# Performance work log

Hardware: AMD Instinct MI355X
Metric: run time of the kernel (lower is better)

Reference implementation:

```python
import jax, jax.numpy as jnp
import numpy as np

FEAT = 128
N_RBF = 20
CUTOFF = 5.0
N_GRAPHS = 128
ATOMS = 64
N_ATOMS = N_GRAPHS * ATOMS  # 8192
N_EDGES = N_ATOMS * 32      # 262144


def setup_inputs() -> dict:
    key = jax.random.key(0)
    ks = jax.random.split(key, 12)
    s_j = jax.random.normal(ks[0], (N_ATOMS, FEAT), jnp.float32)
    v_j = jax.random.normal(ks[1], (N_ATOMS, FEAT, 3), jnp.float32)
    r_ij = jax.random.normal(ks[2], (N_EDGES, 3), jnp.float32) * 1.5
    nbrs = jax.random.randint(ks[3], (N_EDGES, 2), 0, N_ATOMS, dtype=jnp.int32)
    num_atoms = jnp.full((N_GRAPHS,), ATOMS, dtype=jnp.int32)
    sc = 0.05
    W1 = jax.random.normal(ks[4], (FEAT, FEAT), jnp.float32) * sc
    b1 = jnp.zeros((FEAT,), jnp.float32)
    W2 = jax.random.normal(ks[5], (FEAT, 3 * FEAT), jnp.float32) * sc
    b2 = jnp.zeros((3 * FEAT,), jnp.float32)
    Wr = jax.random.normal(ks[6], (N_RBF, 3 * FEAT), jnp.float32) * sc
    br = jnp.zeros((3 * FEAT,), jnp.float32)
    Wd = jax.random.normal(ks[7], (FEAT, 3 * FEAT), jnp.float32) * sc
    bd = jnp.zeros((3 * FEAT,), jnp.float32)
    return {"s_j": s_j, "v_j": v_j, "r_ij": r_ij, "nbrs": nbrs,
            "num_atoms": num_atoms, "W1": W1, "b1": b1, "W2": W2, "b2": b2,
            "Wr": Wr, "br": br, "Wd": Wd, "bd": bd}


def _forward(s_j, v_j, r_ij, nbrs, W1, b1, W2, b2, Wr, br, Wd, bd):
    # preprocess_r
    dist = jnp.linalg.norm(r_ij, axis=-1)            # [E]
    unit = r_ij / dist[:, None]                      # [E,3]

    # InvariantMessage: per-atom MLP, gather at nbrs[:,1], times radial filter
    phi = jax.nn.silu(s_j @ W1 + b1) @ W2 + b2       # [N, 3F]
    phi_e = phi[nbrs[:, 1]]                          # [E, 3F]
    n = jnp.arange(1, N_RBF + 1, dtype=jnp.float32)
    rbf = jnp.sin(n[None, :] * jnp.pi * dist[:, None] / CUTOFF) / dist[:, None]  # [E, n_rbf]
    env = jnp.where(dist < CUTOFF, 0.5 * (jnp.cos(jnp.pi * dist / CUTOFF) + 1.0), 0.0)
    w_s = (rbf @ Wr + br) * env[:, None]             # [E, 3F]
    inv_out = (phi_e * w_s).reshape(-1, 3, FEAT)     # [E, 3, F]

    split_0 = inv_out[:, 0, :][..., None]            # [E, F, 1]
    split_1 = inv_out[:, 1, :]                       # [E, F]
    split_2 = inv_out[:, 2, :][..., None]            # [E, F, 1]

    unit_add = split_2 * unit[:, None, :]            # [E, F, 3]
    delta_v_ij = unit_add + split_0 * v_j[nbrs[:, 1]]  # [E, F, 3]
    delta_s_ij = split_1                             # [E, F]

    seg = nbrs[:, 0]
    delta_v_i = jax.ops.segment_sum(delta_v_ij, seg, num_segments=N_ATOMS)
    delta_s_l = jax.ops.segment_sum(delta_s_ij, seg, num_segments=N_ATOMS)

    # NonLocalInteraction: per-graph exact softmax attention (uniform graph size)
    qkv = s_j @ Wd + bd                              # [N, 3F]
    Q, K, V = jnp.split(qkv, 3, axis=-1)
    Qb = Q.reshape(N_GRAPHS, ATOMS, FEAT)
    Kb = K.reshape(N_GRAPHS, ATOMS, FEAT)
    Vb = V.reshape(N_GRAPHS, ATOMS, FEAT)
    scores = jnp.einsum('bqf,bkf->bqk', Qb, Kb) / jnp.sqrt(jnp.float32(FEAT))
    att = jnp.einsum('bqk,bkf->bqf', jax.nn.softmax(scores, axis=-1), Vb)
    delta_s_nl = att.reshape(N_ATOMS, FEAT)

    delta_s_i = delta_s_l + delta_s_nl
    return delta_s_i, delta_v_i


def reference(s_j, v_j, r_ij, nbrs, num_atoms, W1, b1, W2, b2, Wr, br, Wd, bd):
    # num_atoms is uniform (ATOMS per graph); attention is batched accordingly.
    return _forward(s_j, v_j, r_ij, nbrs, W1, b1, W2, b2, Wr, br, Wd, bd)
```

## Files before the change

kernel.cpp:

```cpp
#include <hip/hip_runtime.h>
#include <hip/hip_bf16.h>
#include <cstdint>

#define FEAT    128
#define NRBF    20
#define NATOMS  8192
#define NEDGES  262144
#define NGRAPH  128
#define APG     64
#define PI_F    3.14159265358979323846f
#define CUTOFF_F 5.0f
#define QTUS    ((size_t)NATOMS * 32 * 6)
#define APW     8

typedef unsigned int uint_t;
typedef unsigned short ushort_t;
typedef __attribute__((ext_vector_type(4))) float f32x4;
typedef __attribute__((ext_vector_type(4))) short short4v;
typedef __attribute__((ext_vector_type(8))) short short8;
struct U3 { uint_t x, y, z; };

__device__ __forceinline__ float bflo(uint_t u) { return __uint_as_float(u << 16); }
__device__ __forceinline__ float bfhi(uint_t u) { return __uint_as_float(u & 0xffff0000u); }
__device__ __forceinline__ float bfus(ushort_t u) { return __uint_as_float((uint_t)u << 16); }
__device__ __forceinline__ ushort_t f2bf(float f) {
  uint_t u = __float_as_uint(f);
  return (ushort_t)((u + 0x7fffu + ((u >> 16) & 1u)) >> 16);
}
__device__ __forceinline__ uint_t pack2(float lo, float hi) {
  return (uint_t)f2bf(lo) | ((uint_t)f2bf(hi) << 16);
}

__device__ __forceinline__ ushort_t swz_elem(const float* __restrict__ W, int N,
                                             int NT, int i) {
  int jj = i & 7, lane = (i >> 3) & 63, tile = i >> 9;
  int ks = tile / NT, ctg = tile - ks * NT;
  int g = lane >> 4, q = lane & 15;
  int k = 32 * ks + 4 * g + (jj & 3) + 16 * (jj >> 2);
  int c = 16 * ctg + q;
  return f2bf(W[(size_t)k * N + c]);
}

__global__ void prep_kernel(const float* __restrict__ v_j, const float* __restrict__ W1,
                            const float* __restrict__ W2, const float* __restrict__ Wd,
                            const float* __restrict__ Wr, const float* __restrict__ br,
                            ushort_t* __restrict__ PV, ushort_t* __restrict__ w1s,
                            ushort_t* __restrict__ w2s, ushort_t* __restrict__ wds,
                            ushort_t* __restrict__ wrs) {
  int i = blockIdx.x * 256 + threadIdx.x;
  if (i < NATOMS * FEAT) {
    int j = i >> 7, f = i & 127;
    int tbl = f >> 5, fl = f & 31;
    const float* vp = v_j + (size_t)i * 3;
    uint_t* o = reinterpret_cast<uint_t*>(PV + (size_t)tbl * QTUS + ((size_t)j * 32 + fl) * 6);
    o[0] = 0u;
    o[1] = pack2(0.f, vp[0]);
    o[2] = pack2(vp[1], vp[2]);
    return;
  }
  i -= NATOMS * FEAT;
  if (i < 16384) { w1s[i] = swz_elem(W1, 128, 8, i); return; }
  i -= 16384;
  if (i < 49152) { w2s[i] = swz_elem(W2, 384, 24, i); return; }
  i -= 49152;
  if (i < 49152) { wds[i] = swz_elem(Wd, 384, 24, i); return; }
  i -= 49152;
  if (i < 12288) {
    int jj = i & 7, lane = (i >> 3) & 63, ct = i >> 9;
    int g = lane >> 4, q = lane & 15;
    int k = 4 * g + (jj & 3) + 16 * (jj >> 2);
    int f = 16 * ct + q;
    float v = (k < NRBF) ? Wr[k * 384 + f] : (k == NRBF ? br[f] : 0.f);
    wrs[i] = f2bf(v);
  }
}

__global__ __launch_bounds__(256) void gemm_fused12(
    const float* __restrict__ s_j, const ushort_t* __restrict__ w1s,
    const float* __restrict__ b1, const ushort_t* __restrict__ w2s,
    const float* __restrict__ b2, ushort_t* __restrict__ PV) {
  __shared__ ushort_t As[64][136];
  __shared__ ushort_t Hs[64][136];
  const int t = threadIdx.x;
  const int r0 = blockIdx.x * 64;
  const int w = t >> 6, l = t & 63, g = l >> 4, q = l & 15;

  for (int i = t; i < 64 * 32; i += 256) {
    int r = i >> 5, k4 = i & 31;
    float4 v = *reinterpret_cast<const float4*>(s_j + (size_t)(r0 + r) * 128 + 4 * k4);
    ushort4 o = {f2bf(v.x), f2bf(v.y), f2bf(v.z), f2bf(v.w)};
    *reinterpret_cast<ushort4*>(&As[r][4 * k4]) = o;
  }
  __syncthreads();

  short8 afr[4];
  #pragma unroll
  for (int ks = 0; ks < 4; ++ks) {
    const ushort_t* ap = &As[16 * w + q][32 * ks + 4 * g];
    short4v alo = *reinterpret_cast<const short4v*>(ap);
    short4v ahi = *reinterpret_cast<const short4v*>(ap + 16);
    afr[ks] = short8{alo[0], alo[1], alo[2], alo[3], ahi[0], ahi[1], ahi[2], ahi[3]};
  }
  #pragma unroll
  for (int ct = 0; ct < 8; ++ct) {
    f32x4 acc = {};
    #pragma unroll
    for (int ks = 0; ks < 4; ++ks) {
      short8 bf = *reinterpret_cast<const short8*>(
          w1s + ((size_t)(ks * 8 + ct) * 64 + l) * 8);
      acc = __builtin_amdgcn_mfma_f32_16x16x32_bf16(afr[ks], bf, acc, 0, 0, 0);
    }
    float bb = b1[16 * ct + q];
    #pragma unroll
    for (int r = 0; r < 4; ++r) {
      float o = acc[r] + bb;
      o = o / (1.f + __expf(-o));
      Hs[16 * w + 4 * g + r][16 * ct + q] = f2bf(o);
    }
  }
  __syncthreads();

  short8 hfr[4];
  #pragma unroll
  for (int ks = 0; ks < 4; ++ks) {
    const ushort_t* ap = &Hs[16 * w + q][32 * ks + 4 * g];
    short4v alo = *reinterpret_cast<const short4v*>(ap);
    short4v ahi = *reinterpret_cast<const short4v*>(ap + 16);
    hfr[ks] = short8{alo[0], alo[1], alo[2], alo[3], ahi[0], ahi[1], ahi[2], ahi[3]};
  }
  for (int cb = 0; cb < 6; ++cb) {
    #pragma unroll
    for (int ct = 0; ct < 4; ++ct) {
      f32x4 acc = {};
      #pragma unroll
      for (int ks = 0; ks < 4; ++ks) {
        short8 bf = *reinterpret_cast<const short8*>(
            w2s + ((size_t)(ks * 24 + cb * 4 + ct) * 64 + l) * 8);
        acc = __builtin_amdgcn_mfma_f32_16x16x32_bf16(hfr[ks], bf, acc, 0, 0, 0);
      }
      int col = cb * 64 + 16 * ct + q;
      float bb = b2[col];
      int f = col & 127, s = col >> 7;
      int tbl = f >> 5, fl = f & 31;
      #pragma unroll
      for (int r = 0; r < 4; ++r) {
        float o = acc[r] + bb;
        int row = r0 + 16 * w + 4 * g + r;
        PV[(size_t)tbl * QTUS + ((size_t)row * 32 + fl) * 6 + s] = f2bf(o);
      }
    }
  }
}

__global__ __launch_bounds__(256) void gemm_mfma(
    const void* __restrict__ Asrc, int a_f32, const ushort_t* __restrict__ Wswz,
    const float* __restrict__ bias, int N, int NT, int silu, int omode,
    void* __restrict__ p0, void* __restrict__ p1) {
  __shared__ ushort_t As[64][136];
  const int t = threadIdx.x;
  const int r0 = blockIdx.x * 64, c0 = blockIdx.y * 64;
  const int w = t >> 6, l = t & 63, g = l >> 4, q = l & 15;

  short8 bf[4][4];
  #pragma unroll
  for (int ks = 0; ks < 4; ++ks)
    #pragma unroll
    for (int ct = 0; ct < 4; ++ct)
      bf[ks][ct] = *reinterpret_cast<const short8*>(
          Wswz + ((size_t)(ks * NT + (c0 >> 4) + ct) * 64 + l) * 8);

  if (a_f32) {
    const float* Af = (const float*)Asrc;
    for (int i = t; i < 64 * 32; i += 256) {
      int r = i >> 5, k4 = i & 31;
      float4 v = *reinterpret_cast<const float4*>(Af + (size_t)(r0 + r) * 128 + 4 * k4);
      ushort4 o = {f2bf(v.x), f2bf(v.y), f2bf(v.z), f2bf(v.w)};
      *reinterpret_cast<ushort4*>(&As[r][4 * k4]) = o;
    }
  } else {
    const ushort_t* Ab = (const ushort_t*)Asrc;
    for (int i = t; i < 64 * 16; i += 256) {
      int r = i >> 4, g8 = i & 15;
      short8 v = *reinterpret_cast<const short8*>(Ab + (size_t)(r0 + r) * 128 + 8 * g8);
      *reinterpret_cast<short8*>(&As[r][8 * g8]) = v;
    }
  }
  __syncthreads();

  f32x4 acc[4] = {};
  #pragma unroll
  for (int ks = 0; ks < 4; ++ks) {
    const ushort_t* ap = &As[16 * w + q][32 * ks + 4 * g];
    short4v alo = *reinterpret_cast<const short4v*>(ap);
    short4v ahi = *reinterpret_cast<const short4v*>(ap + 16);
    short8 af;
    af[0] = alo[0]; af[1] = alo[1]; af[2] = alo[2]; af[3] = alo[3];
    af[4] = ahi[0]; af[5] = ahi[1]; af[6] = ahi[2]; af[7] = ahi[3];
    #pragma unroll
    for (int ct = 0; ct < 4; ++ct)
      acc[ct] = __builtin_amdgcn_mfma_f32_16x16x32_bf16(af, bf[ks][ct], acc[ct], 0, 0, 0);
  }

  #pragma unroll
  for (int ct = 0; ct < 4; ++ct) {
    int col = c0 + 16 * ct + q;
    float bb = bias[col];
    #pragma unroll
    for (int r = 0; r < 4; ++r) {
      float o = acc[ct][r] + bb;
      if (silu) o = o / (1.f + __expf(-o));
      int row = r0 + 16 * w + 4 * g + r;
      if (omode == 1) {
        ((ushort_t*)p0)[(size_t)row * N + col] = f2bf(o);
      } else {
        if (col < 128) ((float*)p0)[(size_t)row * 128 + col] = o;
        else           ((ushort_t*)p1)[(size_t)row * 256 + col - 128] = f2bf(o);
      }
    }
  }
}

__global__ void hist_kernel(const int* __restrict__ nbrs, int* __restrict__ counts) {
  int e = blockIdx.x * blockDim.x + threadIdx.x;
  if (e < NEDGES) atomicAdd(&counts[nbrs[2 * e]], 1);
}

__global__ __launch_bounds__(1024) void scan_kernel(
    const int* __restrict__ counts, int* __restrict__ offs, int* __restrict__ cursor) {
  __shared__ int part[1024];
  const int t = threadIdx.x;
  int local[8];
  int s = 0;
  #pragma unroll
  for (int i = 0; i < 8; ++i) { local[i] = counts[t * 8 + i]; s += local[i]; }
  part[t] = s;
  __syncthreads();
  for (int off = 1; off < 1024; off <<= 1) {
    int v = part[t];
    int add = (t >= off) ? part[t - off] : 0;
    __syncthreads();
    part[t] = v + add;
    __syncthreads();
  }
  int excl = part[t] - s;
  #pragma unroll
  for (int i = 0; i < 8; ++i) {
    offs[t * 8 + i] = excl;
    cursor[t * 8 + i] = excl;
    excl += local[i];
  }
  if (t == 1023) offs[NATOMS] = excl;
}

__global__ void scatter_kernel(const int* __restrict__ nbrs, const float* __restrict__ r_ij,
                               int* __restrict__ cursor, uint4* __restrict__ erec) {
  int e = blockIdx.x * blockDim.x + threadIdx.x;
  if (e < NEDGES) {
    int2 nb = *reinterpret_cast<const int2*>(nbrs + 2 * e);
    int pos = atomicAdd(&cursor[nb.x], 1);
    const float* rp = r_ij + 3 * e;
    erec[pos] = make_uint4((uint_t)nb.y, __float_as_uint(rp[0]),
                           __float_as_uint(rp[1]), __float_as_uint(rp[2]));
  }
}

__global__ __launch_bounds__(256) void edge_mfma8(
    const uint4* __restrict__ erec, const int* __restrict__ offs,
    const ushort_t* __restrict__ PV, const ushort_t* __restrict__ wrs,
    float* __restrict__ out_s, float* __restrict__ out_v) {
  __shared__ short8 sW[6 * 64];
  const int t = threadIdx.x;
  const int qtr = blockIdx.x & 3;
  for (int i = t; i < 6 * 64; i += 256) {
    int tl = i >> 6, l2 = i & 63;
    int s = tl >> 1, c = tl & 1;
    sW[i] = *reinterpret_cast<const short8*>(
        wrs + ((size_t)(s * 8 + 2 * qtr + c) * 64 + l2) * 8);
  }
  __syncthreads();

  const int w = t >> 6, l = t & 63, g = l >> 4, q = l & 15;
  const int a0 = ((blockIdx.x >> 2) * 4 + w) * APW;
  const float c1 = PI_F / CUTOFF_F;
  const char* PVb = reinterpret_cast<const char*>(PV) + (size_t)qtr * QTUS * 2;

  int eb = offs[a0];
  int end = offs[a0 + 1];
  uint4 er = make_uint4(0u, 0u, 0u, 0u);
  if (eb + q < end) er = erec[eb + q];

  for (int aidx = 0; aidx < APW; ++aidx) {
    const int end_next = (aidx + 1 < APW) ? offs[a0 + aidx + 2] : 0;
    float ds0 = 0.f, ds1 = 0.f;
    float dv[2][3] = {};

    for (;;) {
      const bool last = (eb + 16 >= end);
      const int neb = last ? end : (eb + 16);
      const int nend = last ? ((aidx + 1 < APW) ? end_next : neb) : end;
      uint4 ern = make_uint4(0u, 0u, 0u, 0u);
      if (neb + q < nend) ern = erec[neb + q];

      float ang = 0.f, ie = 0.f, env = 0.f, u0 = 0.f, u1 = 0.f, u2 = 0.f;
      int jn = 0;
      if (eb + q < end) {
        jn = (int)er.x;
        float x = __uint_as_float(er.y), y = __uint_as_float(er.z), z = __uint_as_float(er.w);
        float d = sqrtf(x * x + y * y + z * z);
        float inv = 1.f / d;
        ang = c1 * d;
        env = (d < CUTOFF_F) ? 0.5f * (__cosf(ang) + 1.f) : 0.f;
        ie = inv * env;
        u0 = x * inv; u1 = y * inv; u2 = z * inv;
      }
      const char* pb[4];
      float ub[4][3];
      #pragma unroll
      for (int r = 0; r < 4; ++r) {
        int src = 4 * g + r;
        int jr = __shfl(jn, src, 64);
        ub[r][0] = __shfl(u0, src, 64);
        ub[r][1] = __shfl(u1, src, 64);
        ub[r][2] = __shfl(u2, src, 64);
        pb[r] = PVb + (size_t)jr * 384 + (size_t)q * 12;
      }
      U3 ld[2][4];
      #pragma unroll
      for (int c = 0; c < 2; ++c)
        #pragma unroll
        for (int r = 0; r < 4; ++r)
          ld[c][r] = *reinterpret_cast<const U3*>(pb[r] + (size_t)c * 192);
      short8 af;
      #pragma unroll
      for (int jj = 0; jj < 8; ++jj) {
        int k = 4 * g + (jj & 3) + 16 * (jj >> 2);
        float v = (k < NRBF) ? ie * __sinf((float)(k + 1) * ang)
                             : (k == NRBF ? env : 0.f);
        af[jj] = (short)f2bf(v);
      }
      #pragma unroll
      for (int c = 0; c < 2; ++c) {
        short8 b0 = sW[(0 * 2 + c) * 64 + l];
        short8 b1 = sW[(1 * 2 + c) * 64 + l];
        short8 b2 = sW[(2 * 2 + c) * 64 + l];
        f32x4 z4 = {0.f, 0.f, 0.f, 0.f};
        f32x4 cs0 = __builtin_amdgcn_mfma_f32_16x16x32_bf16(af, b0, z4, 0, 0, 0);
        f32x4 cs1 = __builtin_amdgcn_mfma_f32_16x16x32_bf16(af, b1, z4, 0, 0, 0);
        f32x4 cs2 = __builtin_amdgcn_mfma_f32_16x16x32_bf16(af, b2, z4, 0, 0, 0);
        #pragma unroll
        for (int r = 0; r < 4; ++r) {
          U3 u = ld[c][r];
          float p0 = bflo(u.x), p1 = bfhi(u.x);
          float p2 = bflo(u.y), v0 = bfhi(u.y);
          float v1 = bflo(u.z), v2 = bfhi(u.z);
          float pw0 = p0 * cs0[r];
          if (c == 0) ds0 += p1 * cs1[r]; else ds1 += p1 * cs1[r];
          float pw2 = p2 * cs2[r];
          dv[c][0] += pw0 * v0 + pw2 * ub[r][0];
          dv[c][1] += pw0 * v1 + pw2 * ub[r][1];
          dv[c][2] += pw0 * v2 + pw2 * ub[r][2];
        }
      }
      er = ern;
      eb = neb;
      if (last) break;
    }

    float r0v = ds0, r1v = ds1;
    r0v += __shfl_xor(r0v, 16, 64); r0v += __shfl_xor(r0v, 32, 64);
    r1v += __shfl_xor(r1v, 16, 64); r1v += __shfl_xor(r1v, 32, 64);
    float dvr[2][3];
    #pragma unroll
    for (int c = 0; c < 2; ++c)
      #pragma unroll
      for (int cc = 0; cc < 3; ++cc) {
        float y = dv[c][cc];
        y += __shfl_xor(y, 16, 64); y += __shfl_xor(y, 32, 64);
        dvr[c][cc] = y;
      }
    if (g < 2) {
      int atom = a0 + aidx;
      float sv = (g == 0) ? r0v : r1v;
      float d0 = (g == 0) ? dvr[0][0] : dvr[1][0];
      float d1 = (g == 0) ? dvr[0][1] : dvr[1][1];
      float d2 = (g == 0) ? dvr[0][2] : dvr[1][2];
      int f = 32 * qtr + 16 * g + q;
      out_s[(size_t)atom * FEAT + f] = sv;
      float* ov = out_v + (size_t)atom * 384 + (size_t)f * 3;
      ov[0] = d0; ov[1] = d1; ov[2] = d2;
    }
    end = end_next;
  }
}

__device__ __forceinline__ float wave_max64(float v) {
  #pragma unroll
  for (int m = 32; m > 0; m >>= 1) v = fmaxf(v, __shfl_xor(v, m, 64));
  return v;
}
__device__ __forceinline__ float wave_sum64(float v) {
  #pragma unroll
  for (int m = 32; m > 0; m >>= 1) v += __shfl_xor(v, m, 64);
  return v;
}

__global__ __launch_bounds__(256) void attn_kernel(const float* __restrict__ Qf,
                                                   const ushort_t* __restrict__ kvbf,
                                                   float* __restrict__ out_s) {
  __shared__ float4 Ks4[64 * 32];
  __shared__ float  Vs[64][130];
  __shared__ float  Ps[4][4][64];
  const int b = blockIdx.x >> 1, half = blockIdx.x & 1;
  const int t = threadIdx.x;
  const float* qbase = Qf + (size_t)b * APG * 128;
  const ushort_t* kvb = kvbf + (size_t)b * APG * 256;

  for (int i = t; i < 64 * 32; i += 256) {
    int a = i >> 5, gg = i & 31;
    ushort4 k4 = *reinterpret_cast<const ushort4*>(kvb + a * 256 + 4 * gg);
    float4 kf = {bfus(k4.x), bfus(k4.y), bfus(k4.z), bfus(k4.w)};
    Ks4[a * 32 + (gg ^ (a & 7))] = kf;
  }
  for (int i = t; i < 64 * 32; i += 256) {
    int a = i >> 5, gg = i & 31;
    ushort4 v4 = *reinterpret_cast<const ushort4*>(kvb + a * 256 + 128 + 4 * gg);
    Vs[a][4 * gg + 0] = bfus(v4.x); Vs[a][4 * gg + 1] = bfus(v4.y);
    Vs[a][4 * gg + 2] = bfus(v4.z); Vs[a][4 * gg + 3] = bfus(v4.w);
  }
  __syncthreads();

  const int w = t >> 6, l = t & 63;
  const float scale = 0.08838834764831845f;

  for (int qq = 8 * half + w; qq < 8 * half + 8; qq += 4) {
    const float* q0p = qbase + (size_t)(4 * qq + 0) * 128;
    const float* q1p = qbase + (size_t)(4 * qq + 1) * 128;
    const float* q2p = qbase + (size_t)(4 * qq + 2) * 128;
    const float* q3p = qbase + (size_t)(4 * qq + 3) * 128;
    float s0 = 0.f, s1 = 0.f, s2 = 0.f, s3 = 0.f;
    #pragma unroll 8
    for (int i = 0; i < 32; ++i) {
      float4 k = Ks4[l * 32 + (i ^ (l & 7))];
      float4 q0 = *reinterpret_cast<const float4*>(q0p + 4 * i);
      float4 q1 = *reinterpret_cast<const float4*>(q1p + 4 * i);
      float4 q2 = *reinterpret_cast<const float4*>(q2p + 4 * i);
      float4 q3 = *reinterpret_cast<const float4*>(q3p + 4 * i);
      s0 += q0.x * k.x + q0.y * k.y + q0.z * k.z + q0.w * k.w;
      s1 += q1.x * k.x + q1.y * k.y + q1.z * k.z + q1.w * k.w;
      s2 += q2.x * k.x + q2.y * k.y + q2.z * k.z + q2.w * k.w;
      s3 += q3.x * k.x + q3.y * k.y + q3.z * k.z + q3.w * k.w;
    }
    s0 *= scale; s1 *= scale; s2 *= scale; s3 *= scale;

    float p0 = __expf(s0 - wave_max64(s0));
    float p1 = __expf(s1 - wave_max64(s1));
    float p2 = __expf(s2 - wave_max64(s2));
    float p3 = __expf(s3 - wave_max64(s3));
    p0 /= wave_sum64(p0); p1 /= wave_sum64(p1);
    p2 /= wave_sum64(p2); p3 /= wave_sum64(p3);

    Ps[w][0][l] = p0; Ps[w][1][l] = p1; Ps[w][2][l] = p2; Ps[w][3][l] = p3;
    __threadfence_block();

    float a00 = 0.f, a01 = 0.f, a10 = 0.f, a11 = 0.f;
    float a20 = 0.f, a21 = 0.f, a30 = 0.f, a31 = 0.f;
    for (int a = 0; a < 64; ++a) {
      float2 v = *reinterpret_cast<const float2*>(&Vs[a][2 * l]);
      float pa0 = Ps[w][0][a], pa1 = Ps[w][1][a];
      float pa2 = Ps[w][2][a], pa3 = Ps[w][3][a];
      a00 += pa0 * v.x; a01 += pa0 * v.y;
      a10 += pa1 * v.x; a11 += pa1 * v.y;
      a20 += pa2 * v.x; a21 += pa2 * v.y;
      a30 += pa3 * v.x; a31 += pa3 * v.y;
    }
    size_t row0 = (size_t)(b * APG + 4 * qq) * FEAT + 2 * l;
    float2* o0 = reinterpret_cast<float2*>(out_s + row0);
    float2* o1 = reinterpret_cast<float2*>(out_s + row0 + FEAT);
    float2* o2 = reinterpret_cast<float2*>(out_s + row0 + 2 * FEAT);
    float2* o3 = reinterpret_cast<float2*>(out_s + row0 + 3 * FEAT);
    float2 c0 = *o0; c0.x += a00; c0.y += a01; *o0 = c0;
    float2 c1 = *o1; c1.x += a10; c1.y += a11; *o1 = c1;
    float2 c2 = *o2; c2.x += a20; c2.y += a21; *o2 = c2;
    float2 c3 = *o3; c3.x += a30; c3.y += a31; *o3 = c3;
    __threadfence_block();
  }
}

extern "C" void kernel_launch(void* const* d_in, const int* in_sizes, int n_in,
                              void* d_out, int out_size, void* d_ws, size_t ws_size,
                              hipStream_t stream) {
  const float* s_j  = (const float*)d_in[0];
  const float* v_j  = (const float*)d_in[1];
  const float* r_ij = (const float*)d_in[2];
  const int*   nbrs = (const int*)d_in[3];
  const float* W1   = (const float*)d_in[5];
  const float* b1   = (const float*)d_in[6];
  const float* W2   = (const float*)d_in[7];
  const float* b2   = (const float*)d_in[8];
  const float* Wr   = (const float*)d_in[9];
  const float* br   = (const float*)d_in[10];
  const float* Wd   = (const float*)d_in[11];
  const float* bd   = (const float*)d_in[12];

  float* out_s = (float*)d_out;
  float* out_v = out_s + (size_t)NATOMS * FEAT;

  float*    Qf   = (float*)d_ws;
  ushort_t* kvbf = (ushort_t*)(Qf + NATOMS * FEAT);
  ushort_t* PV   = kvbf + (size_t)NATOMS * 256;
  ushort_t* w1s  = PV + 4 * QTUS;
  ushort_t* w2s  = w1s + 16384;
  ushort_t* wds  = w2s + 49152;
  ushort_t* wrs  = wds + 49152;
  uint4*    erec = (uint4*)(wrs + 12288);
  int* offs   = (int*)(erec + NEDGES);
  int* cursor = offs + (NATOMS + 1);
  int* counts = cursor + NATOMS;

  int prep_total = NATOMS * FEAT + 16384 + 49152 + 49152 + 12288;
  prep_kernel<<<(prep_total + 255) / 256, 256, 0, stream>>>(
      v_j, W1, W2, Wd, Wr, br, PV, w1s, w2s, wds, wrs);

  gemm_fused12<<<NATOMS / 64, 256, 0, stream>>>(s_j, w1s, b1, w2s, b2, PV);

  hipMemsetAsync(counts, 0, NATOMS * sizeof(int), stream);
  hist_kernel<<<NEDGES / 256, 256, 0, stream>>>(nbrs, counts);
  scan_kernel<<<1, 1024, 0, stream>>>(counts, offs, cursor);
  scatter_kernel<<<NEDGES / 256, 256, 0, stream>>>(nbrs, r_ij, cursor, erec);

  gemm_mfma<<<dim3(NATOMS / 64, 6), 256, 0, stream>>>(
      s_j, 1, wds, bd, 384, 24, 0, 3, Qf, kvbf);

  edge_mfma8<<<NATOMS / APW, 256, 0, stream>>>(erec, offs, PV, wrs, out_s, out_v);
  attn_kernel<<<NGRAPH * 2, 256, 0, stream>>>(Qf, kvbf, out_s);
}
```

Measured before the change: 141.5 us.

## Merge GEMM launches, fold histogram into prep, widen grids for edge and attention

Folds the edge histogram into the prep kernel and merges the phi MLP GEMM and the QKV GEMM into one launch. In the merged launch, blocks with y<6 each compute one 64-column slice of W2 and blocks with y>=6 compute the QKV projection. Because of this split, each phi block recomputes the first-layer SiLU hidden tile, six times redundantly per row block. APW drops from 8 to 4, doubling the edge kernel's grid, and the attention grid grows to 4 blocks per graph so each wave handles one query group. The aim is fewer launches and more parallelism, paid for with duplicated first-layer GEMM work and a K/V tile reload per extra attention block.

```diff
diff --git a/kernel.cpp b/kernel.cpp
--- a/kernel.cpp
+++ b/kernel.cpp
@@ -11,7 +11,7 @@
 #define PI_F    3.14159265358979323846f
 #define CUTOFF_F 5.0f
 #define QTUS    ((size_t)NATOMS * 32 * 6)
-#define APW     8
+#define APW     4
 
 typedef unsigned int uint_t;
 typedef unsigned short ushort_t;
@@ -44,9 +44,10 @@
 __global__ void prep_kernel(const float* __restrict__ v_j, const float* __restrict__ W1,
                             const float* __restrict__ W2, const float* __restrict__ Wd,
                             const float* __restrict__ Wr, const float* __restrict__ br,
+                            const int* __restrict__ nbrs,
                             ushort_t* __restrict__ PV, ushort_t* __restrict__ w1s,
                             ushort_t* __restrict__ w2s, ushort_t* __restrict__ wds,
-                            ushort_t* __restrict__ wrs) {
+                            ushort_t* __restrict__ wrs, int* __restrict__ counts) {
   int i = blockIdx.x * 256 + threadIdx.x;
   if (i < NATOMS * FEAT) {
     int j = i >> 7, f = i & 127;
@@ -72,35 +73,66 @@
     int f = 16 * ct + q;
     float v = (k < NRBF) ? Wr[k * 384 + f] : (k == NRBF ? br[f] : 0.f);
     wrs[i] = f2bf(v);
-  }
-}
-
-__global__ __launch_bounds__(256) void gemm_fused12(
+    return;
+  }
+  i -= 12288;
+  if (i < NEDGES) atomicAdd(&counts[nbrs[2 * i]], 1);
+}
+
+__global__ __launch_bounds__(256) void gemm_big(
     const float* __restrict__ s_j, const ushort_t* __restrict__ w1s,
     const float* __restrict__ b1, const ushort_t* __restrict__ w2s,
-    const float* __restrict__ b2, ushort_t* __restrict__ PV) {
-  __shared__ ushort_t As[64][136];
-  __shared__ ushort_t Hs[64][136];
+    const float* __restrict__ b2, const ushort_t* __restrict__ wds,
+    const float* __restrict__ bd, ushort_t* __restrict__ PV,
+    float* __restrict__ Qf, ushort_t* __restrict__ kvbf) {
+  __shared__ ushort_t Buf[64][136];
   const int t = threadIdx.x;
   const int r0 = blockIdx.x * 64;
+  const int y = blockIdx.y;
   const int w = t >> 6, l = t & 63, g = l >> 4, q = l & 15;
 
   for (int i = t; i < 64 * 32; i += 256) {
     int r = i >> 5, k4 = i & 31;
     float4 v = *reinterpret_cast<const float4*>(s_j + (size_t)(r0 + r) * 128 + 4 * k4);
     ushort4 o = {f2bf(v.x), f2bf(v.y), f2bf(v.z), f2bf(v.w)};
-    *reinterpret_cast<ushort4*>(&As[r][4 * k4]) = o;
+    *reinterpret_cast<ushort4*>(&Buf[r][4 * k4]) = o;
   }
   __syncthreads();
 
   short8 afr[4];
   #pragma unroll
   for (int ks = 0; ks < 4; ++ks) {
-    const ushort_t* ap = &As[16 * w + q][32 * ks + 4 * g];
+    const ushort_t* ap = &Buf[16 * w + q][32 * ks + 4 * g];
     short4v alo = *reinterpret_cast<const short4v*>(ap);
     short4v ahi = *reinterpret_cast<const short4v*>(ap + 16);
     afr[ks] = short8{alo[0], alo[1], alo[2], alo[3], ahi[0], ahi[1], ahi[2], ahi[3]};
   }
+
+  if (y >= 6) {
+    const int yy = y - 6;
+    #pragma unroll
+    for (int ct = 0; ct < 4; ++ct) {
+      f32x4 acc = {};
+      #pragma unroll
+      for (int ks = 0; ks < 4; ++ks) {
+        short8 bf = *reinterpret_cast<const short8*>(
+            wds + ((size_t)(ks * 24 + yy * 4 + ct) * 64 + l) * 8);
+        acc = __builtin_amdgcn_mfma_f32_16x16x32_bf16(afr[ks], bf, acc, 0, 0, 0);
+      }
+      int col = yy * 64 + 16 * ct + q;
+      float bb = bd[col];
+      #pragma unroll
+      for (int r = 0; r < 4; ++r) {
+        float o = acc[r] + bb;
+        int row = r0 + 16 * w + 4 * g + r;
+        if (col < 128) Qf[(size_t)row * 128 + col] = o;
+        else           kvbf[(size_t)row * 256 + col - 128] = f2bf(o);
+      }
+    }
+    return;
+  }
+
+  __syncthreads();
   #pragma unroll
   for (int ct = 0; ct < 8; ++ct) {
     f32x4 acc = {};
@@ -115,7 +147,7 @@
     for (int r = 0; r < 4; ++r) {
       float o = acc[r] + bb;
       o = o / (1.f + __expf(-o));
-      Hs[16 * w + 4 * g + r][16 * ct + q] = f2bf(o);
+      Buf[16 * w + 4 * g + r][16 * ct + q] = f2bf(o);
     }
   }
   __syncthreads();
@@ -123,106 +155,31 @@
   short8 hfr[4];
   #pragma unroll
   for (int ks = 0; ks < 4; ++ks) {
-    const ushort_t* ap = &Hs[16 * w + q][32 * ks + 4 * g];
+    const ushort_t* ap = &Buf[16 * w + q][32 * ks + 4 * g];
     short4v alo = *reinterpret_cast<const short4v*>(ap);
     short4v ahi = *reinterpret_cast<const short4v*>(ap + 16);
     hfr[ks] = short8{alo[0], alo[1], alo[2], alo[3], ahi[0], ahi[1], ahi[2], ahi[3]};
   }
-  for (int cb = 0; cb < 6; ++cb) {
-    #pragma unroll
-    for (int ct = 0; ct < 4; ++ct) {
-      f32x4 acc = {};
-      #pragma unroll
-      for (int ks = 0; ks < 4; ++ks) {
-        short8 bf = *reinterpret_cast<const short8*>(
-            w2s + ((size_t)(ks * 24 + cb * 4 + ct) * 64 + l) * 8);
-        acc = __builtin_amdgcn_mfma_f32_16x16x32_bf16(hfr[ks], bf, acc, 0, 0, 0);
-      }
-      int col = cb * 64 + 16 * ct + q;
-      float bb = b2[col];
-      int f = col & 127, s = col >> 7;
-      int tbl = f >> 5, fl = f & 31;
-      #pragma unroll
-      for (int r = 0; r < 4; ++r) {
-        float o = acc[r] + bb;
-        int row = r0 + 16 * w + 4 * g + r;
-        PV[(size_t)tbl * QTUS + ((size_t)row * 32 + fl) * 6 + s] = f2bf(o);
-      }
-    }
-  }
-}
-
-__global__ __launch_bounds__(256) void gemm_mfma(
-    const void* __restrict__ Asrc, int a_f32, const ushort_t* __restrict__ Wswz,
-    const float* __restrict__ bias, int N, int NT, int silu, int omode,
-    void* __restrict__ p0, void* __restrict__ p1) {
-  __shared__ ushort_t As[64][136];
-  const int t = threadIdx.x;
-  const int r0 = blockIdx.x * 64, c0 = blockIdx.y * 64;
-  const int w = t >> 6, l = t & 63, g = l >> 4, q = l & 15;
-
-  short8 bf[4][4];
-  #pragma unroll
-  for (int ks = 0; ks < 4; ++ks)
-    #pragma unroll
-    for (int ct = 0; ct < 4; ++ct)
-      bf[ks][ct] = *reinterpret_cast<const short8*>(
-          Wswz + ((size_t)(ks * NT + (c0 >> 4) + ct) * 64 + l) * 8);
-
-  if (a_f32) {
-    const float* Af = (const float*)Asrc;
-    for (int i = t; i < 64 * 32; i += 256) {
-      int r = i >> 5, k4 = i & 31;
-      float4 v = *reinterpret_cast<const float4*>(Af + (size_t)(r0 + r) * 128 + 4 * k4);
-      ushort4 o = {f2bf(v.x), f2bf(v.y), f2bf(v.z), f2bf(v.w)};
-      *reinterpret_cast<ushort4*>(&As[r][4 * k4]) = o;
-    }
-  } else {
-    const ushort_t* Ab = (const ushort_t*)Asrc;
-    for (int i = t; i < 64 * 16; i += 256) {
-      int r = i >> 4, g8 = i & 15;
-      short8 v = *reinterpret_cast<const short8*>(Ab + (size_t)(r0 + r) * 128 + 8 * g8);
-      *reinterpret_cast<short8*>(&As[r][8 * g8]) = v;
-    }
-  }
-  __syncthreads();
-
-  f32x4 acc[4] = {};
-  #pragma unroll
-  for (int ks = 0; ks < 4; ++ks) {
-    const ushort_t* ap = &As[16 * w + q][32 * ks + 4 * g];
-    short4v alo = *reinterpret_cast<const short4v*>(ap);
-    short4v ahi = *reinterpret_cast<const short4v*>(ap + 16);
-    short8 af;
-    af[0] = alo[0]; af[1] = alo[1]; af[2] = alo[2]; af[3] = alo[3];
-    af[4] = ahi[0]; af[5] = ahi[1]; af[6] = ahi[2]; af[7] = ahi[3];
-    #pragma unroll
-    for (int ct = 0; ct < 4; ++ct)
-      acc[ct] = __builtin_amdgcn_mfma_f32_16x16x32_bf16(af, bf[ks][ct], acc[ct], 0, 0, 0);
-  }
-
   #pragma unroll
   for (int ct = 0; ct < 4; ++ct) {
-    int col = c0 + 16 * ct + q;
-    float bb = bias[col];
+    f32x4 acc = {};
+    #pragma unroll
+    for (int ks = 0; ks < 4; ++ks) {
+      short8 bf = *reinterpret_cast<const short8*>(
+          w2s + ((size_t)(ks * 24 + y * 4 + ct) * 64 + l) * 8);
+      acc = __builtin_amdgcn_mfma_f32_16x16x32_bf16(hfr[ks], bf, acc, 0, 0, 0);
+    }
+    int col = y * 64 + 16 * ct + q;
+    float bb = b2[col];
+    int f = col & 127, s = col >> 7;
+    int tbl = f >> 5, fl = f & 31;
     #pragma unroll
     for (int r = 0; r < 4; ++r) {
-      float o = acc[ct][r] + bb;
-      if (silu) o = o / (1.f + __expf(-o));
+      float o = acc[r] + bb;
       int row = r0 + 16 * w + 4 * g + r;
-      if (omode == 1) {
-        ((ushort_t*)p0)[(size_t)row * N + col] = f2bf(o);
-      } else {
-        if (col < 128) ((float*)p0)[(size_t)row * 128 + col] = o;
-        else           ((ushort_t*)p1)[(size_t)row * 256 + col - 128] = f2bf(o);
-      }
-    }
-  }
-}
-
-__global__ void hist_kernel(const int* __restrict__ nbrs, int* __restrict__ counts) {
-  int e = blockIdx.x * blockDim.x + threadIdx.x;
-  if (e < NEDGES) atomicAdd(&counts[nbrs[2 * e]], 1);
+      PV[(size_t)tbl * QTUS + ((size_t)row * 32 + fl) * 6 + s] = f2bf(o);
+    }
+  }
 }
 
 __global__ __launch_bounds__(1024) void scan_kernel(
@@ -410,7 +367,7 @@
   __shared__ float4 Ks4[64 * 32];
   __shared__ float  Vs[64][130];
   __shared__ float  Ps[4][4][64];
-  const int b = blockIdx.x >> 1, half = blockIdx.x & 1;
+  const int b = blockIdx.x >> 2, quad = blockIdx.x & 3;
   const int t = threadIdx.x;
   const float* qbase = Qf + (size_t)b * APG * 128;
   const ushort_t* kvb = kvbf + (size_t)b * APG * 256;
@@ -430,60 +387,58 @@
   __syncthreads();
 
   const int w = t >> 6, l = t & 63;
+  const int qq = 4 * quad + w;
   const float scale = 0.08838834764831845f;
 
-  for (int qq = 8 * half + w; qq < 8 * half + 8; qq += 4) {
-    const float* q0p = qbase + (size_t)(4 * qq + 0) * 128;
-    const float* q1p = qbase + (size_t)(4 * qq + 1) * 128;
-    const float* q2p = qbase + (size_t)(4 * qq + 2) * 128;
-    const float* q3p = qbase + (size_t)(4 * qq + 3) * 128;
-    float s0 = 0.f, s1 = 0.f, s2 = 0.f, s3 = 0.f;
-    #pragma unroll 8
-    for (int i = 0; i < 32; ++i) {
-      float4 k = Ks4[l * 32 + (i ^ (l & 7))];
-      float4 q0 = *reinterpret_cast<const float4*>(q0p + 4 * i);
-      float4 q1 = *reinterpret_cast<const float4*>(q1p + 4 * i);
-      float4 q2 = *reinterpret_cast<const float4*>(q2p + 4 * i);
-      float4 q3 = *reinterpret_cast<const float4*>(q3p + 4 * i);
-      s0 += q0.x * k.x + q0.y * k.y + q0.z * k.z + q0.w * k.w;
-      s1 += q1.x * k.x + q1.y * k.y + q1.z * k.z + q1.w * k.w;
-      s2 += q2.x * k.x + q2.y * k.y + q2.z * k.z + q2.w * k.w;
-      s3 += q3.x * k.x + q3.y * k.y + q3.z * k.z + q3.w * k.w;
-    }
-    s0 *= scale; s1 *= scale; s2 *= scale; s3 *= scale;
-
-    float p0 = __expf(s0 - wave_max64(s0));
-    float p1 = __expf(s1 - wave_max64(s1));
-    float p2 = __expf(s2 - wave_max64(s2));
-    float p3 = __expf(s3 - wave_max64(s3));
-    p0 /= wave_sum64(p0); p1 /= wave_sum64(p1);
-    p2 /= wave_sum64(p2); p3 /= wave_sum64(p3);
-
-    Ps[w][0][l] = p0; Ps[w][1][l] = p1; Ps[w][2][l] = p2; Ps[w][3][l] = p3;
-    __threadfence_block();
-
-    float a00 = 0.f, a01 = 0.f, a10 = 0.f, a11 = 0.f;
-    float a20 = 0.f, a21 = 0.f, a30 = 0.f, a31 = 0.f;
-    for (int a = 0; a < 64; ++a) {
-      float2 v = *reinterpret_cast<const float2*>(&Vs[a][2 * l]);
-      float pa0 = Ps[w][0][a], pa1 = Ps[w][1][a];
-      float pa2 = Ps[w][2][a], pa3 = Ps[w][3][a];
-      a00 += pa0 * v.x; a01 += pa0 * v.y;
-      a10 += pa1 * v.x; a11 += pa1 * v.y;
-      a20 += pa2 * v.x; a21 += pa2 * v.y;
-      a30 += pa3 * v.x; a31 += pa3 * v.y;
-    }
-    size_t row0 = (size_t)(b * APG + 4 * qq) * FEAT + 2 * l;
-    float2* o0 = reinterpret_cast<float2*>(out_s + row0);
-    float2* o1 = reinterpret_cast<float2*>(out_s + row0 + FEAT);
-    float2* o2 = reinterpret_cast<float2*>(out_s + row0 + 2 * FEAT);
-    float2* o3 = reinterpret_cast<float2*>(out_s + row0 + 3 * FEAT);
-    float2 c0 = *o0; c0.x += a00; c0.y += a01; *o0 = c0;
-    float2 c1 = *o1; c1.x += a10; c1.y += a11; *o1 = c1;
-    float2 c2 = *o2; c2.x += a20; c2.y += a21; *o2 = c2;
-    float2 c3 = *o3; c3.x += a30; c3.y += a31; *o3 = c3;
-    __threadfence_block();
-  }
+  const float* q0p = qbase + (size_t)(4 * qq + 0) * 128;
+  const float* q1p = qbase + (size_t)(4 * qq + 1) * 128;
+  const float* q2p = qbase + (size_t)(4 * qq + 2) * 128;
+  const float* q3p = qbase + (size_t)(4 * qq + 3) * 128;
+  float s0 = 0.f, s1 = 0.f, s2 = 0.f, s3 = 0.f;
+  #pragma unroll 8
+  for (int i = 0; i < 32; ++i) {
+    float4 k = Ks4[l * 32 + (i ^ (l & 7))];
+    float4 q0 = *reinterpret_cast<const float4*>(q0p + 4 * i);
+    float4 q1 = *reinterpret_cast<const float4*>(q1p + 4 * i);
+    float4 q2 = *reinterpret_cast<const float4*>(q2p + 4 * i);
+    float4 q3 = *reinterpret_cast<const float4*>(q3p + 4 * i);
+    s0 += q0.x * k.x + q0.y * k.y + q0.z * k.z + q0.w * k.w;
+    s1 += q1.x * k.x + q1.y * k.y + q1.z * k.z + q1.w * k.w;
+    s2 += q2.x * k.x + q2.y * k.y + q2.z * k.z + q2.w * k.w;
+    s3 += q3.x * k.x + q3.y * k.y + q3.z * k.z + q3.w * k.w;
+  }
+  s0 *= scale; s1 *= scale; s2 *= scale; s3 *= scale;
+
+  float p0 = __expf(s0 - wave_max64(s0));
+  float p1 = __expf(s1 - wave_max64(s1));
+  float p2 = __expf(s2 - wave_max64(s2));
+  float p3 = __expf(s3 - wave_max64(s3));
+  p0 /= wave_sum64(p0); p1 /= wave_sum64(p1);
+  p2 /= wave_sum64(p2); p3 /= wave_sum64(p3);
+
+  Ps[w][0][l] = p0; Ps[w][1][l] = p1; Ps[w][2][l] = p2; Ps[w][3][l] = p3;
+  __threadfence_block();
+
+  float a00 = 0.f, a01 = 0.f, a10 = 0.f, a11 = 0.f;
+  float a20 = 0.f, a21 = 0.f, a30 = 0.f, a31 = 0.f;
+  for (int a = 0; a < 64; ++a) {
+    float2 v = *reinterpret_cast<const float2*>(&Vs[a][2 * l]);
+    float pa0 = Ps[w][0][a], pa1 = Ps[w][1][a];
+    float pa2 = Ps[w][2][a], pa3 = Ps[w][3][a];
+    a00 += pa0 * v.x; a01 += pa0 * v.y;
+    a10 += pa1 * v.x; a11 += pa1 * v.y;
+    a20 += pa2 * v.x; a21 += pa2 * v.y;
+    a30 += pa3 * v.x; a31 += pa3 * v.y;
+  }
+  size_t row0 = (size_t)(b * APG + 4 * qq) * FEAT + 2 * l;
+  float2* o0 = reinterpret_cast<float2*>(out_s + row0);
+  float2* o1 = reinterpret_cast<float2*>(out_s + row0 + FEAT);
+  float2* o2 = reinterpret_cast<float2*>(out_s + row0 + 2 * FEAT);
+  float2* o3 = reinterpret_cast<float2*>(out_s + row0 + 3 * FEAT);
+  float2 c0 = *o0; c0.x += a00; c0.y += a01; *o0 = c0;
+  float2 c1 = *o1; c1.x += a10; c1.y += a11; *o1 = c1;
+  float2 c2 = *o2; c2.x += a20; c2.y += a21; *o2 = c2;
+  float2 c3 = *o3; c3.x += a30; c3.y += a31; *o3 = c3;
 }
 
 extern "C" void kernel_launch(void* const* d_in, const int* in_sizes, int n_in,
@@ -517,20 +472,18 @@
   int* cursor = offs + (NATOMS + 1);
   int* counts = cursor + NATOMS;
 
-  int prep_total = NATOMS * FEAT + 16384 + 49152 + 49152 + 12288;
+  hipMemsetAsync(counts, 0, NATOMS * sizeof(int), stream);
+
+  int prep_total = NATOMS * FEAT + 16384 + 49152 + 49152 + 12288 + NEDGES;
   prep_kernel<<<(prep_total + 255) / 256, 256, 0, stream>>>(
-      v_j, W1, W2, Wd, Wr, br, PV, w1s, w2s, wds, wrs);
-
-  gemm_fused12<<<NATOMS / 64, 256, 0, stream>>>(s_j, w1s, b1, w2s, b2, PV);
-
-  hipMemsetAsync(counts, 0, NATOMS * sizeof(int), stream);
-  hist_kernel<<<NEDGES / 256, 256, 0, stream>>>(nbrs, counts);
+      v_j, W1, W2, Wd, Wr, br, nbrs, PV, w1s, w2s, wds, wrs, counts);
+
   scan_kernel<<<1, 1024, 0, stream>>>(counts, offs, cursor);
   scatter_kernel<<<NEDGES / 256, 256, 0, stream>>>(nbrs, r_ij, cursor, erec);
 
-  gemm_mfma<<<dim3(NATOMS / 64, 6), 256, 0, stream>>>(
-      s_j, 1, wds, bd, 384, 24, 0, 3, Qf, kvbf);
+  gemm_big<<<dim3(NATOMS / 64, 12), 256, 0, stream>>>(
+      s_j, w1s, b1, w2s, b2, wds, bd, PV, Qf, kvbf);
 
   edge_mfma8<<<NATOMS / APW, 256, 0, stream>>>(erec, offs, PV, wrs, out_s, out_v);
-  attn_kernel<<<NGRAPH * 2, 256, 0, stream>>>(Qf, kvbf, out_s);
-}
+  attn_kernel<<<NGRAPH * 4, 256, 0, stream>>>(Qf, kvbf, out_s);
+}
```

Result: faster. 131.1 us (-7.3%).
